# Optimization experiments

Measured on AMD Instinct MI355X. Metric: run time of the kernel, lower is better.

## Reference

```python
import jax, jax.numpy as jnp
import numpy as np

NUM_HEADS = 16
WINDOW = 128

def setup_inputs() -> dict:
    key = jax.random.key(0)
    ks = jax.random.split(key, 9)
    E, B, S = 1024, 2, 2048
    sc = 1.0 / np.sqrt(E)
    return {
        'x':  jax.random.normal(ks[0], (B, S, E), jnp.float32),
        'Wq': jax.random.normal(ks[1], (E, E), jnp.float32) * sc,
        'bq': jax.random.normal(ks[2], (E,), jnp.float32) * 0.02,
        'Wk': jax.random.normal(ks[3], (E, E), jnp.float32) * sc,
        'bk': jax.random.normal(ks[4], (E,), jnp.float32) * 0.02,
        'Wv': jax.random.normal(ks[5], (E, E), jnp.float32) * sc,
        'bv': jax.random.normal(ks[6], (E,), jnp.float32) * 0.02,
        'Wo': jax.random.normal(ks[7], (E, E), jnp.float32) * sc,
        'bo': jax.random.normal(ks[8], (E,), jnp.float32) * 0.02,
    }

def reference(x, Wq, bq, Wk, bk, Wv, bv, Wo, bo):
    B, S, E = x.shape
    H = NUM_HEADS
    D = E // H
    # projections -> [B, H, S, D]
    q = (x @ Wq + bq).reshape(B, S, H, D).transpose(0, 2, 1, 3)
    k = (x @ Wk + bk).reshape(B, S, H, D).transpose(0, 2, 1, 3)
    v = (x @ Wv + bv).reshape(B, S, H, D).transpose(0, 2, 1, 3)
    # dense scores [B, H, S, S]
    energy = jnp.einsum('bhqd,bhkd->bhqk', q, k)
    idx = jnp.arange(S)
    blocked = jnp.abs(idx[:, None] - idx[None, :]) > WINDOW  # True = outside band
    neg = jnp.finfo(jnp.float32).min
    energy = jnp.where(blocked[None, None], neg, energy)
    # note: original scales by sqrt(emb_size), not sqrt(head_dim)
    att = jax.nn.softmax(energy / jnp.sqrt(jnp.float32(E)), axis=-1)
    out = jnp.einsum('bhqk,bhkd->bhqd', att, v)
    out = out.transpose(0, 2, 1, 3).reshape(B, S, E)
    return out @ Wo + bo
```

## Files before the change

### kernel.cpp

```cpp
#include <hip/hip_runtime.h>

typedef unsigned short u16;
typedef unsigned int u32;
typedef __attribute__((ext_vector_type(8))) short bf16x8;
typedef __attribute__((ext_vector_type(4))) float f32x4;
typedef __attribute__((ext_vector_type(4))) unsigned int u32x4;
typedef __attribute__((ext_vector_type(4))) unsigned short u16x4;

#define DEV static __device__ __forceinline__

DEV u16 f2bf(float f) {
  unsigned u = __builtin_bit_cast(unsigned, f);
  u += 0x7FFFu + ((u >> 16) & 1u);
  return (u16)(u >> 16);
}

DEV u32 cvt_pk_bf16(float lo, float hi) {
  u32 d;
  asm("v_cvt_pk_bf16_f32 %0, %1, %2" : "=v"(d) : "v"(lo), "v"(hi));
  return d;
}

DEV void load_lds16(const void* g, void* l) {
  __builtin_amdgcn_global_load_lds(
      (const __attribute__((address_space(1))) unsigned int*)g,
      (__attribute__((address_space(3))) unsigned int*)l, 16, 0, 0);
}


__global__ void k_prep(const float* __restrict__ x,
                       const float* __restrict__ bq, const float* __restrict__ bk,
                       const float* __restrict__ bv,
                       const float* __restrict__ Wq, const float* __restrict__ Wk,
                       const float* __restrict__ Wv, const float* __restrict__ Wo,
                       u16* __restrict__ xb, u16* __restrict__ wtqkv,
                       u16* __restrict__ wto, float* __restrict__ bias) {
  const int tid = threadIdx.x;
  const int bid = blockIdx.x;
  if (bid < 4096) {
    __shared__ float t[32][33];
    const int wi = bid >> 10, inner = bid & 1023;
    const float* W = (wi == 0) ? Wq : (wi == 1) ? Wk : (wi == 2) ? Wv : Wo;
    u16* Wt = (wi == 3) ? wto : wtqkv + (size_t)wi * 1024 * 1024;
    const int tx = tid & 31, ty = tid >> 5;
    const int c0 = (inner & 31) * 32, r0 = (inner >> 5) * 32;
#pragma unroll
    for (int i = 0; i < 4; ++i)
      t[ty + i * 8][tx] = W[(size_t)(r0 + ty + i * 8) * 1024 + c0 + tx];
    __syncthreads();
#pragma unroll
    for (int i = 0; i < 4; ++i)
      Wt[(size_t)(c0 + ty + i * 8) * 1024 + r0 + tx] = f2bf(t[tx][ty + i * 8]);
  } else if (bid < 8192) {
    int i = ((bid - 4096) * 256 + tid) * 4;
    f32x4 v = *(const f32x4*)(x + i);
    u16x4 o;
#pragma unroll
    for (int j = 0; j < 4; ++j) o[j] = f2bf(v[j]);
    *(u16x4*)(xb + i) = o;
  } else {
    int i = (bid - 8192) * 256 + tid;
    float v = (i < 1024) ? bq[i] : (i < 2048) ? bk[i - 1024] : bv[i - 2048];
    bias[i] = v;
  }
}


template <int BN, typename CT>
__launch_bounds__(256, 2) __global__
void k_gemm_bt(const u16* __restrict__ A, const u16* __restrict__ Bt,
               const float* __restrict__ bias, CT* __restrict__ C, int ldc,
               u16* __restrict__ vtp) {
  constexpr int BM = 128, BK = 64;
  constexpr int NJ = BN / 32;
  constexpr int EPW = BN / 2 + 4;
  constexpr int HALF = (BM + BN) * BK * 2;
  constexpr int LPS = BM / 32 + BN / 32;
  __shared__ __align__(16) char smem[2 * HALF];
  float (*ep)[16][EPW] = (float (*)[16][EPW])smem;

  const int tid = threadIdx.x;
  const int w = tid >> 6, lane = tid & 63, g = lane >> 4, n16 = lane & 15;
  const int wm = w >> 1, wn = w & 1;

  const int nbx = gridDim.x;
  const int flat = blockIdx.y * nbx + blockIdx.x;
  const int cpx = (nbx * gridDim.y) >> 3;
  const int swz = (flat & 7) * cpx + (flat >> 3);
  const int m0 = (swz / nbx) * BM, n0 = (swz % nbx) * BN;

#define STAGE(k0, bsel)                                                        \
  do {                                                                         \
    u16* lAb = (u16*)(smem + (bsel) * HALF);                                   \
    u16* lBb = lAb + BM * BK;                                                  \
    _Pragma("unroll")                                                          \
    for (int r = 0; r < BM / 32; ++r) {                                        \
      int s = r * 256 + tid;                                                   \
      int row = s >> 3, cc = (s & 7) ^ (row & 7);                              \
      load_lds16(A + (size_t)(m0 + row) * 1024 + (k0) + cc * 8, lAb + s * 8);  \
    }                                                                          \
    _Pragma("unroll")                                                          \
    for (int r = 0; r < BN / 32; ++r) {                                        \
      int s = r * 256 + tid;                                                   \
      int row = s >> 3, cc = (s & 7) ^ (row & 7);                              \
      load_lds16(Bt + (size_t)(n0 + row) * 1024 + (k0) + cc * 8, lBb + s * 8); \
    }                                                                          \
  } while (0)

  f32x4 acc[4][NJ] = {};
  STAGE(0, 0);
  STAGE(64, 1);
#pragma unroll 2
  for (int t = 0; t < 16; ++t) {
    const int buf = t & 1;
    if (t < 15) {
      asm volatile("s_waitcnt vmcnt(%0)" ::"n"(LPS) : "memory");
    } else {
      asm volatile("s_waitcnt vmcnt(0)" ::: "memory");
    }
    __builtin_amdgcn_s_barrier();
    const u16* lAb = (const u16*)(smem + buf * HALF);
    const u16* lBb = lAb + BM * BK;
    bf16x8 af[2][4], bfr[2][NJ];
#pragma unroll
    for (int kh = 0; kh < 2; ++kh) {
      const int csel = ((kh * 4 + g) ^ (n16 & 7)) * 8;
#pragma unroll
      for (int i = 0; i < 4; ++i)
        af[kh][i] = *(const bf16x8*)&lAb[(wm * 64 + i * 16 + n16) * 64 + csel];
#pragma unroll
      for (int j = 0; j < NJ; ++j)
        bfr[kh][j] = *(const bf16x8*)&lBb[(wn * (BN / 2) + j * 16 + n16) * 64 + csel];
    }
    asm volatile("s_waitcnt lgkmcnt(0)" ::: "memory");
    __builtin_amdgcn_s_barrier();
    if (t < 14) STAGE((t + 2) * 64, buf);
    __builtin_amdgcn_s_setprio(1);
#pragma unroll
    for (int kh = 0; kh < 2; ++kh)
#pragma unroll
      for (int i = 0; i < 4; ++i)
#pragma unroll
        for (int j = 0; j < NJ; ++j)
          acc[i][j] =
              __builtin_amdgcn_mfma_f32_16x16x32_bf16(af[kh][i], bfr[kh][j], acc[i][j], 0, 0, 0);
    __builtin_amdgcn_s_setprio(0);
  }
#undef STAGE
  __syncthreads();

  const int m_base = m0 + wm * 64, n_base = n0 + wn * (BN / 2);
  bool vmode = false;
  if constexpr (sizeof(CT) == 2 && BN == 128)
    vmode = (vtp != nullptr) && (n_base >= 2048);

#pragma unroll
  for (int i = 0; i < 4; ++i) {
#pragma unroll
    for (int j = 0; j < NJ; ++j) {
      float bv = bias[n_base + j * 16 + n16];
#pragma unroll
      for (int jj = 0; jj < 4; ++jj)
        ep[w][g * 4 + jj][j * 16 + n16] = acc[i][j][jj] + bv;
    }
    asm volatile("s_waitcnt lgkmcnt(0)" ::: "memory");
    if (vmode) {
      const int head = (n_base - 2048) >> 6;
      const int m_row0 = m_base + i * 16;
      const int bb = m_row0 >> 11, s0 = m_row0 & 2047;
      union { u16 a[16]; u32x4 v[2]; } pk;
#pragma unroll
      for (int r = 0; r < 16; ++r) pk.a[r] = f2bf(ep[w][r][lane]);
      size_t vrow = ((size_t)(bb * 16 + head) * 64 + lane) * 2048 + s0;
      *(u32x4*)(vtp + vrow) = pk.v[0];
      *(u32x4*)(vtp + vrow + 8) = pk.v[1];
    } else {
      constexpr int CPR = BN / 8;
      constexpr int P = 16 * CPR / 64;
#pragma unroll
      for (int p = 0; p < P; ++p) {
        int fl = p * 64 + lane;
        int row = fl / CPR, cc = (fl % CPR) * 4;
        f32x4 v = *(const f32x4*)&ep[w][row][cc];
        size_t off = (size_t)(m_base + i * 16 + row) * ldc + n_base + cc;
        if constexpr (sizeof(CT) == 2) {
          u16x4 o;
#pragma unroll
          for (int q = 0; q < 4; ++q) o[q] = f2bf(v[q]);
          *(u16x4*)(C + off) = o;
        } else {
          *(f32x4*)(C + off) = v;
        }
      }
    }
    asm volatile("s_waitcnt lgkmcnt(0)" ::: "memory");
  }
}


__launch_bounds__(256, 3) __global__
void k_attn(const u16* __restrict__ qkv, const u16* __restrict__ vt,
            u16* __restrict__ attn) {
  __shared__ __align__(16) u16 KV[20480];
  __shared__ __align__(16) u16 Ostg[4][16][64];
  const int tid = threadIdx.x;
  const int w = tid >> 6, lane = tid & 63, g = lane >> 4, n16 = lane & 15;
  const int bid = (blockIdx.x & 7) * 128 + (blockIdx.x >> 3);
  const int qt = bid & 31, h = (bid >> 5) & 15, b = bid >> 9;
  const int q0b = qt * 64;
  const int kvb = q0b - 128;
  const int q0 = q0b + w * 16;
  const int kv0 = q0 - 128;
  const int q = q0 + n16;
  const int bh = b * 16 + h;

  {
    const u16* kpart = qkv + (size_t)b * 2048 * 3072 + 1024 + h * 64;
#pragma unroll
    for (int i = 0; i < 10; ++i) {
      int c = i * 256 + tid;
      int r = c >> 3, sl = c & 7;
      int m = (r & 3) | (((r >> 3) & 1) << 2);
      int srcr = min(max(kvb + r, 0), 2047);
      load_lds16(kpart + (size_t)srcr * 3072 + (sl ^ m) * 8, &KV[c * 8]);
    }
  }

  const size_t rowQ = (size_t)(b * 2048 + q) * 3072 + h * 64;
  bf16x8 qf0 = *(const bf16x8*)(qkv + rowQ + g * 8);
  bf16x8 qf1 = *(const bf16x8*)(qkv + rowQ + 32 + g * 8);
  __syncthreads();

  const int kbase = 8 * (n16 >> 2) + (n16 & 3);
  const int wrel = 16 * w;
  f32x4 sv[18];
#pragma unroll
  for (int t = 0; t < 18; ++t) {
    int kr = wrel + 32 * (t >> 1) + 4 * (t & 1) + kbase;
    int krl = min(kr, 319);
    int p = (krl & 3) | (((krl >> 3) & 1) << 2);
    const u16* kp = &KV[krl * 64];
    bf16x8 kf0 = *(const bf16x8*)(kp + (g ^ p) * 8);
    bf16x8 kf1 = *(const bf16x8*)(kp + ((g + 4) ^ p) * 8);
    f32x4 s = {0.f, 0.f, 0.f, 0.f};
    s = __builtin_amdgcn_mfma_f32_16x16x32_bf16(kf0, qf0, s, 0, 0, 0);
    s = __builtin_amdgcn_mfma_f32_16x16x32_bf16(kf1, qf1, s, 0, 0, 0);
    sv[t] = s;
  }
  __syncthreads();

  {
    const u16* vpart = vt + (size_t)bh * 64 * 2048;
#pragma unroll
    for (int i = 0; i < 10; ++i) {
      int c = i * 256 + tid;
      int d = c / 40, cc = c - d * 40;
      int j = cc ^ (d & 7);
      int srck = min(max(kvb + j * 8, 0), 2040);
      load_lds16(vpart + (size_t)d * 2048 + srck, &KV[c * 8]);
    }
  }

  const float NEG = -__builtin_inff();
#pragma unroll
  for (int t = 0; t < 18; ++t) {
    int kb = kv0 + 32 * (t >> 1) + 4 * (t & 1) + 8 * g;
#pragma unroll
    for (int jj = 0; jj < 4; ++jj) {
      int k = kb + jj;
      bool ok = ((unsigned)k < 2048u) && ((unsigned)(q - k + 128) <= 256u);
      sv[t][jj] = ok ? sv[t][jj] : NEG;
    }
  }

  float mx = NEG;
#pragma unroll
  for (int t = 0; t < 18; ++t)
    mx = fmaxf(mx, fmaxf(fmaxf(sv[t][0], sv[t][1]), fmaxf(sv[t][2], sv[t][3])));
  mx = fmaxf(mx, __shfl_xor(mx, 16));
  mx = fmaxf(mx, __shfl_xor(mx, 32));

  const float c = 0.04508422017f;
  const float nmc = -mx * c;
  float sum = 0.f;
#pragma unroll
  for (int t = 0; t < 18; ++t)
#pragma unroll
    for (int jj = 0; jj < 4; ++jj) {
      float p = exp2f(fmaf(sv[t][jj], c, nmc));
      sv[t][jj] = p;
      sum += p;
    }
  sum += __shfl_xor(sum, 16);
  sum += __shfl_xor(sum, 32);
  const float inv = 1.f / sum;

  __syncthreads();

  f32x4 oacc[4] = {};
#pragma unroll
  for (int s = 0; s < 9; ++s) {
    union { u32 u[4]; bf16x8 v; } paf;
    paf.u[0] = cvt_pk_bf16(sv[2 * s][0], sv[2 * s][1]);
    paf.u[1] = cvt_pk_bf16(sv[2 * s][2], sv[2 * s][3]);
    paf.u[2] = cvt_pk_bf16(sv[2 * s + 1][0], sv[2 * s + 1][1]);
    paf.u[3] = cvt_pk_bf16(sv[2 * s + 1][2], sv[2 * s + 1][3]);
    int jc = min(2 * w + 4 * s + g, 39);
#pragma unroll
    for (int dt = 0; dt < 4; ++dt) {
      int d = dt * 16 + n16;
      bf16x8 vf = *(const bf16x8*)&KV[d * 320 + (jc ^ (d & 7)) * 8];
      oacc[dt] = __builtin_amdgcn_mfma_f32_16x16x32_bf16(paf.v, vf, oacc[dt], 0, 0, 0);
    }
  }

  float rs[4];
#pragma unroll
  for (int jj = 0; jj < 4; ++jj) rs[jj] = __shfl(inv, 4 * g + jj);

#pragma unroll
  for (int dt = 0; dt < 4; ++dt)
#pragma unroll
    for (int jj = 0; jj < 4; ++jj)
      Ostg[w][g * 4 + jj][dt * 16 + n16] = f2bf(oacc[dt][jj] * rs[jj]);
  asm volatile("s_waitcnt lgkmcnt(0)" ::: "memory");
#pragma unroll
  for (int p = 0; p < 2; ++p) {
    int fl = p * 512 + lane * 8;
    int row = fl >> 6, col = fl & 63;
    u32x4 v = *(const u32x4*)&Ostg[w][row][col];
    *(u32x4*)(attn + (size_t)(b * 2048 + q0 + row) * 1024 + h * 64 + col) = v;
  }
}


extern "C" void kernel_launch(void* const* d_in, const int* in_sizes, int n_in,
                              void* d_out, int out_size, void* d_ws, size_t ws_size,
                              hipStream_t stream) {
  const float* x  = (const float*)d_in[0];
  const float* Wq = (const float*)d_in[1];
  const float* bq = (const float*)d_in[2];
  const float* Wk = (const float*)d_in[3];
  const float* bk = (const float*)d_in[4];
  const float* Wv = (const float*)d_in[5];
  const float* bv = (const float*)d_in[6];
  const float* Wo = (const float*)d_in[7];
  const float* bo = (const float*)d_in[8];

  char* ws = (char*)d_ws;
  const size_t MB = 1ull << 20;
  u16*   xb    = (u16*)(ws + 0);
  u16*   wtqkv = (u16*)(ws + 8 * MB);
  u16*   wto   = (u16*)(ws + 14 * MB);
  float* bias  = (float*)(ws + 16 * MB);
  u16*   qkvb  = (u16*)(ws + 17 * MB);
  u16*   vtb   = (u16*)(ws + 41 * MB);
  u16*   attnb = (u16*)(ws + 0);

  k_prep<<<8204, 256, 0, stream>>>(x, bq, bk, bv, Wq, Wk, Wv, Wo,
                                   xb, wtqkv, wto, bias);
  k_gemm_bt<128, u16><<<dim3(24, 32), 256, 0, stream>>>(xb, wtqkv, bias, qkvb, 3072, vtb);
  k_attn<<<1024, 256, 0, stream>>>(qkvb, vtb, attnb);
  k_gemm_bt<64, float><<<dim3(16, 32), 256, 0, stream>>>(attnb, wto, bo, (float*)d_out,
                                                         1024, nullptr);
}
```

Baseline: 74.04 us.

## Deepen GEMM pipeline to four BK=32 stages; drop softmax max and sum via MFMA

Result: slower. 80.46 us (+8.7%).

```diff
diff --git a/kernel.cpp b/kernel.cpp
--- a/kernel.cpp
+++ b/kernel.cpp
@@ -71,12 +71,12 @@
 void k_gemm_bt(const u16* __restrict__ A, const u16* __restrict__ Bt,
                const float* __restrict__ bias, CT* __restrict__ C, int ldc,
                u16* __restrict__ vtp) {
-  constexpr int BM = 128, BK = 64;
+  constexpr int BM = 128, BK = 32;
   constexpr int NJ = BN / 32;
   constexpr int EPW = BN / 2 + 4;
   constexpr int HALF = (BM + BN) * BK * 2;
-  constexpr int LPS = BM / 32 + BN / 32;
-  __shared__ __align__(16) char smem[2 * HALF];
+  constexpr int LPS = BM / 64 + BN / 64;
+  __shared__ __align__(16) char smem[4 * HALF];
   float (*ep)[16][EPW] = (float (*)[16][EPW])smem;
 
   const int tid = threadIdx.x;
@@ -94,58 +94,58 @@
     u16* lAb = (u16*)(smem + (bsel) * HALF);                                   \
     u16* lBb = lAb + BM * BK;                                                  \
     _Pragma("unroll")                                                          \
-    for (int r = 0; r < BM / 32; ++r) {                                        \
+    for (int r = 0; r < BM / 64; ++r) {                                        \
       int s = r * 256 + tid;                                                   \
-      int row = s >> 3, cc = (s & 7) ^ (row & 7);                              \
+      int row = s >> 2, cc = (s & 3) ^ (row & 3);                              \
       load_lds16(A + (size_t)(m0 + row) * 1024 + (k0) + cc * 8, lAb + s * 8);  \
     }                                                                          \
     _Pragma("unroll")                                                          \
-    for (int r = 0; r < BN / 32; ++r) {                                        \
+    for (int r = 0; r < BN / 64; ++r) {                                        \
       int s = r * 256 + tid;                                                   \
-      int row = s >> 3, cc = (s & 7) ^ (row & 7);                              \
+      int row = s >> 2, cc = (s & 3) ^ (row & 3);                              \
       load_lds16(Bt + (size_t)(n0 + row) * 1024 + (k0) + cc * 8, lBb + s * 8); \
     }                                                                          \
   } while (0)
 
+#define KITER(T, VMC, DOSTAGE)                                                 \
+  do {                                                                         \
+    asm volatile("s_waitcnt vmcnt(%0)" ::"n"(VMC) : "memory");                 \
+    __builtin_amdgcn_s_barrier();                                              \
+    const u16* lAb = (const u16*)(smem + ((T) & 3) * HALF);                    \
+    const u16* lBb = lAb + BM * BK;                                            \
+    const int csel = (g ^ (n16 & 3)) * 8;                                      \
+    bf16x8 af[4], bfr[NJ];                                                     \
+    _Pragma("unroll")                                                          \
+    for (int i = 0; i < 4; ++i)                                                \
+      af[i] = *(const bf16x8*)&lAb[(wm * 64 + i * 16 + n16) * 32 + csel];      \
+    _Pragma("unroll")                                                          \
+    for (int j = 0; j < NJ; ++j)                                               \
+      bfr[j] = *(const bf16x8*)&lBb[(wn * (BN / 2) + j * 16 + n16) * 32 + csel]; \
+    asm volatile("s_waitcnt lgkmcnt(0)" ::: "memory");                         \
+    __builtin_amdgcn_s_barrier();                                              \
+    if (DOSTAGE) STAGE(((T) + 4) * 32, (T) & 3);                               \
+    __builtin_amdgcn_s_setprio(1);                                             \
+    _Pragma("unroll")                                                          \
+    for (int i = 0; i < 4; ++i)                                                \
+      _Pragma("unroll")                                                        \
+      for (int j = 0; j < NJ; ++j)                                             \
+        acc[i][j] =                                                            \
+            __builtin_amdgcn_mfma_f32_16x16x32_bf16(af[i], bfr[j], acc[i][j], 0, 0, 0); \
+    __builtin_amdgcn_s_setprio(0);                                             \
+  } while (0)
+
   f32x4 acc[4][NJ] = {};
   STAGE(0, 0);
-  STAGE(64, 1);
-#pragma unroll 2
-  for (int t = 0; t < 16; ++t) {
-    const int buf = t & 1;
-    if (t < 15) {
-      asm volatile("s_waitcnt vmcnt(%0)" ::"n"(LPS) : "memory");
-    } else {
-      asm volatile("s_waitcnt vmcnt(0)" ::: "memory");
-    }
-    __builtin_amdgcn_s_barrier();
-    const u16* lAb = (const u16*)(smem + buf * HALF);
-    const u16* lBb = lAb + BM * BK;
-    bf16x8 af[2][4], bfr[2][NJ];
-#pragma unroll
-    for (int kh = 0; kh < 2; ++kh) {
-      const int csel = ((kh * 4 + g) ^ (n16 & 7)) * 8;
-#pragma unroll
-      for (int i = 0; i < 4; ++i)
-        af[kh][i] = *(const bf16x8*)&lAb[(wm * 64 + i * 16 + n16) * 64 + csel];
-#pragma unroll
-      for (int j = 0; j < NJ; ++j)
-        bfr[kh][j] = *(const bf16x8*)&lBb[(wn * (BN / 2) + j * 16 + n16) * 64 + csel];
-    }
-    asm volatile("s_waitcnt lgkmcnt(0)" ::: "memory");
-    __builtin_amdgcn_s_barrier();
-    if (t < 14) STAGE((t + 2) * 64, buf);
-    __builtin_amdgcn_s_setprio(1);
-#pragma unroll
-    for (int kh = 0; kh < 2; ++kh)
-#pragma unroll
-      for (int i = 0; i < 4; ++i)
-#pragma unroll
-        for (int j = 0; j < NJ; ++j)
-          acc[i][j] =
-              __builtin_amdgcn_mfma_f32_16x16x32_bf16(af[kh][i], bfr[kh][j], acc[i][j], 0, 0, 0);
-    __builtin_amdgcn_s_setprio(0);
-  }
+  STAGE(32, 1);
+  STAGE(64, 2);
+  STAGE(96, 3);
+#pragma unroll 4
+  for (int t = 0; t < 28; ++t) KITER(t, 3 * LPS, true);
+  KITER(28, 3 * LPS, false);
+  KITER(29, 2 * LPS, false);
+  KITER(30, 1 * LPS, false);
+  KITER(31, 0, false);
+#undef KITER
 #undef STAGE
   __syncthreads();
 
@@ -262,42 +262,24 @@
   }
 
   const float NEG = -__builtin_inff();
+  const int lo = max(q - 128, 0);
+  const unsigned rng = (unsigned)(min(q + 128, 2047) - lo);
+  const float c = 0.04508422017f;
 #pragma unroll
   for (int t = 0; t < 18; ++t) {
-    int kb = kv0 + 32 * (t >> 1) + 4 * (t & 1) + 8 * g;
+    int kb = kv0 + 32 * (t >> 1) + 4 * (t & 1) + 8 * g - lo;
 #pragma unroll
     for (int jj = 0; jj < 4; ++jj) {
-      int k = kb + jj;
-      bool ok = ((unsigned)k < 2048u) && ((unsigned)(q - k + 128) <= 256u);
-      sv[t][jj] = ok ? sv[t][jj] : NEG;
-    }
-  }
-
-  float mx = NEG;
-#pragma unroll
-  for (int t = 0; t < 18; ++t)
-    mx = fmaxf(mx, fmaxf(fmaxf(sv[t][0], sv[t][1]), fmaxf(sv[t][2], sv[t][3])));
-  mx = fmaxf(mx, __shfl_xor(mx, 16));
-  mx = fmaxf(mx, __shfl_xor(mx, 32));
-
-  const float c = 0.04508422017f;
-  const float nmc = -mx * c;
-  float sum = 0.f;
-#pragma unroll
-  for (int t = 0; t < 18; ++t)
-#pragma unroll
-    for (int jj = 0; jj < 4; ++jj) {
-      float p = exp2f(fmaf(sv[t][jj], c, nmc));
-      sv[t][jj] = p;
-      sum += p;
-    }
-  sum += __shfl_xor(sum, 16);
-  sum += __shfl_xor(sum, 32);
-  const float inv = 1.f / sum;
+      bool ok = (unsigned)(kb + jj) <= rng;
+      sv[t][jj] = exp2f((ok ? sv[t][jj] : NEG) * c);
+    }
+  }
 
   __syncthreads();
 
+  const bf16x8 ones = {0x3F80, 0x3F80, 0x3F80, 0x3F80, 0x3F80, 0x3F80, 0x3F80, 0x3F80};
   f32x4 oacc[4] = {};
+  f32x4 osum = {};
 #pragma unroll
   for (int s = 0; s < 9; ++s) {
     union { u32 u[4]; bf16x8 v; } paf;
@@ -312,17 +294,18 @@
       bf16x8 vf = *(const bf16x8*)&KV[d * 320 + (jc ^ (d & 7)) * 8];
       oacc[dt] = __builtin_amdgcn_mfma_f32_16x16x32_bf16(paf.v, vf, oacc[dt], 0, 0, 0);
     }
-  }
-
-  float rs[4];
-#pragma unroll
-  for (int jj = 0; jj < 4; ++jj) rs[jj] = __shfl(inv, 4 * g + jj);
+    osum = __builtin_amdgcn_mfma_f32_16x16x32_bf16(paf.v, ones, osum, 0, 0, 0);
+  }
+
+  float inv[4];
+#pragma unroll
+  for (int jj = 0; jj < 4; ++jj) inv[jj] = 1.f / osum[jj];
 
 #pragma unroll
   for (int dt = 0; dt < 4; ++dt)
 #pragma unroll
     for (int jj = 0; jj < 4; ++jj)
-      Ostg[w][g * 4 + jj][dt * 16 + n16] = f2bf(oacc[dt][jj] * rs[jj]);
+      Ostg[w][g * 4 + jj][dt * 16 + n16] = f2bf(oacc[dt][jj] * inv[jj]);
   asm volatile("s_waitcnt lgkmcnt(0)" ::: "memory");
 #pragma unroll
   for (int p = 0; p < 2; ++p) {
```
